# Optimization experiments

Hardware: AMD Instinct MI355X
Metric: run time of the kernel (lower is better)

## Reference

```python
import jax, jax.numpy as jnp
import numpy as np

B, S, D, W, P = 32, 512, 768, 256, 1024


def setup_inputs() -> dict:
    key = jax.random.key(0)
    k_h, k_len, k_pair, k_w1, k_w2 = jax.random.split(key, 5)
    h = jax.random.normal(k_h, (B, S, D), dtype=jnp.float32)
    # ragged word spans: each word covers 1 or 2 contiguous subwords; total <= S
    word_len = jax.random.randint(k_len, (B, W), 1, 3, dtype=jnp.int32)  # in {1,2}
    word_start = jnp.concatenate(
        [jnp.zeros((B, 1), jnp.int32), jnp.cumsum(word_len, axis=1)[:, :-1]], axis=1
    )
    # word-index pairs per configuration; -1 means "use zero embedding"
    pair_idx = jax.random.randint(k_pair, (B, P, 2), 0, W + 1, dtype=jnp.int32) - 1
    w1 = jax.random.normal(k_w1, (2 * D, 300), dtype=jnp.float32) * 0.02
    b1 = jnp.zeros((300,), jnp.float32)
    w2 = jax.random.normal(k_w2, (300, 4), dtype=jnp.float32) * 0.02
    b2 = jnp.zeros((4,), jnp.float32)
    return {"h": h, "w1": w1, "b1": b1, "w2": w2, "b2": b2,
            "word_start": word_start, "word_len": word_len, "pair_idx": pair_idx}


def reference(h, w1, b1, w2, b2, word_start, word_len, pair_idx):
    # --- mean-pool subword embeddings per word via prefix sums (segment mean) ---
    csum = jnp.cumsum(h, axis=1)                                   # [B,S,D]
    csum = jnp.concatenate([jnp.zeros_like(csum[:, :1]), csum], 1)  # [B,S+1,D]
    end = word_start + word_len                                     # [B,W]
    seg_sum = (jnp.take_along_axis(csum, end[:, :, None], axis=1)
               - jnp.take_along_axis(csum, word_start[:, :, None], axis=1))
    word_emb = seg_sum / word_len[:, :, None].astype(h.dtype)       # [B,W,D]
    # --- per-pair gather with -1 -> zero vector ---
    valid = (pair_idx >= 0)                                         # [B,P,2]
    idx = jnp.maximum(pair_idx, 0).reshape(h.shape[0], -1)          # [B,2P]
    emb = jnp.take_along_axis(word_emb, idx[:, :, None], axis=1)    # [B,2P,D]
    emb = emb.reshape(pair_idx.shape[0], pair_idx.shape[1], 2, -1)
    emb = jnp.where(valid[..., None], emb, jnp.zeros((), h.dtype))
    mlp_input = emb.reshape(-1, 2 * h.shape[-1])                    # [B*P, 2D]
    # --- tiny MLP + softmax (dropout is identity in eval) ---
    x = jnp.tanh(mlp_input @ w1 + b1)
    return jax.nn.softmax(x @ w2 + b2, axis=-1)                     # [B*P, 4]
```

## Files before the change

kernel.cpp:

```cpp
#include <hip/hip_runtime.h>
#include <cstddef>
#include <cstdint>

#define Bb   32
#define Ss   512
#define Dd   768
#define Ww   256
#define Pp   1024
#define NH   300
#define SLOT1 320
#define NPAD 640
#define Mm   (Bb * Ww)
#define ZROW 8192
#define ZOFF (ZROW * NPAD)
#define PBUF ((Mm + 1) * NPAD)
#define KH   384
#define NST  12

typedef __attribute__((ext_vector_type(8))) short bf16x8;
typedef __attribute__((ext_vector_type(4))) float f32x4;

#define GPTR(p) ((const __attribute__((address_space(1))) void*)(p))
#define LPTR(p) ((__attribute__((address_space(3))) void*)(p))

__device__ __forceinline__ unsigned short f2bf(float x) {
    unsigned u = __builtin_bit_cast(unsigned, x);
    u += 0x7fffu + ((u >> 16) & 1u);
    return (unsigned short)(u >> 16);
}
__device__ __forceinline__ float bf2f(unsigned short u) {
    return __builtin_bit_cast(float, (unsigned)u << 16);
}
__device__ __forceinline__ float fast_tanh(float x) {
    x = fminf(fmaxf(x, -15.0f), 15.0f);
    float e = __expf(2.0f * x);
    return 1.0f - 2.0f * __builtin_amdgcn_rcpf(e + 1.0f);
}

__global__ __launch_bounds__(256) void prep_kernel(
    const float* __restrict__ h, const float* __restrict__ w1,
    const int* __restrict__ word_start, const int* __restrict__ word_len,
    unsigned short* __restrict__ emb, unsigned short* __restrict__ bmatT,
    unsigned short* __restrict__ proj)
{
    const int gid    = blockIdx.x * 256 + threadIdx.x;
    const int stride = 1024 * 256;

    for (int u = gid; u < Mm * 192; u += stride) {
        const int m = u / 192;
        const int c = u - m * 192;
        const int b   = m >> 8;
        const int s0  = word_start[m];
        const int len = word_len[m];
        const float* p = h + (size_t)b * (Ss * Dd) + (size_t)s0 * Dd + c * 4;
        float4 v = *(const float4*)p;
        if (len == 2) {
            float4 v2 = *(const float4*)(p + Dd);
            v.x = (v.x + v2.x) * 0.5f;
            v.y = (v.y + v2.y) * 0.5f;
            v.z = (v.z + v2.z) * 0.5f;
            v.w = (v.w + v2.w) * 0.5f;
        }
        ushort4 o = make_ushort4(f2bf(v.x), f2bf(v.y), f2bf(v.z), f2bf(v.w));
        *(ushort4*)(emb + (size_t)m * Dd + c * 4) = o;
    }

    for (int u = gid; u < Dd * NPAD; u += stride) {
        const int k = u / NPAD;
        const int n = u - k * NPAD;
        float v = 0.0f;
        if (n < NH)                            v = w1[(size_t)k * NH + n];
        else if (n >= SLOT1 && n < SLOT1 + NH) v = w1[(size_t)(Dd + k) * NH + (n - SLOT1)];
        bmatT[(size_t)n * Dd + k] = f2bf(v);
    }

    if (gid < NPAD / 4) {
        *(ushort4*)(proj + ZOFF + gid * 4)        = make_ushort4(0, 0, 0, 0);
        *(ushort4*)(proj + PBUF + ZOFF + gid * 4) = make_ushort4(0, 0, 0, 0);
    }
}

__global__ __launch_bounds__(256) void gemm_kernel(
    const unsigned short* __restrict__ emb, const unsigned short* __restrict__ bmatT,
    unsigned short* __restrict__ proj)
{
    __shared__ bf16x8 Al[3][4][128];
    __shared__ bf16x8 Bl[3][4][128];

    const int bid = blockIdx.x;
    const int t   = threadIdx.x;

    const int swz   = (bid & 7) * 80 + (bid >> 3);
    const int kh    = swz / 320;
    const int tIdx  = swz - kh * 320;
    const int mBase = (tIdx / 5) * 128;
    const int nBase = (tIdx % 5) * 128;
    const int kOff  = kh * KH;

    const int srow = t & 127;
    const int skb8 = (t >> 7) << 3;
    const unsigned short* srcA = emb   + (size_t)(mBase + srow) * Dd + kOff + skb8;
    const unsigned short* srcB = bmatT + (size_t)(nBase + srow) * Dd + kOff + skb8;
    char* ldsA = (char*)&Al[0][0][0] + t * 16;
    char* ldsB = (char*)&Bl[0][0][0] + t * 16;

    const int lane = t & 63;
    const int w    = t >> 6;
    const int wr   = w >> 1;
    const int wc   = w & 1;
    const int fr   = lane & 15;
    const int kb   = lane >> 4;

    f32x4 acc[4][4];
#pragma unroll
    for (int i = 0; i < 4; ++i)
#pragma unroll
        for (int j = 0; j < 4; ++j)
#pragma unroll
            for (int r = 0; r < 4; ++r) acc[i][j][r] = 0.0f;

#define STAGE(c, off)                                                                          \
    __builtin_amdgcn_global_load_lds(GPTR(srcA + (off)),      LPTR(ldsA + (c) * 8192),        16, 0, 0); \
    __builtin_amdgcn_global_load_lds(GPTR(srcA + (off) + 16), LPTR(ldsA + (c) * 8192 + 4096), 16, 0, 0); \
    __builtin_amdgcn_global_load_lds(GPTR(srcB + (off)),      LPTR(ldsB + (c) * 8192),        16, 0, 0); \
    __builtin_amdgcn_global_load_lds(GPTR(srcB + (off) + 16), LPTR(ldsB + (c) * 8192 + 4096), 16, 0, 0)

#define COMPUTE(c)                                                                             \
    {                                                                                          \
        bf16x8 a[4], b[4];                                                                     \
        _Pragma("unroll")                                                                      \
        for (int mi = 0; mi < 4; ++mi) a[mi] = Al[c][kb][wr * 64 + mi * 16 + fr];              \
        _Pragma("unroll")                                                                      \
        for (int ni = 0; ni < 4; ++ni) b[ni] = Bl[c][kb][wc * 64 + ni * 16 + fr];              \
        _Pragma("unroll")                                                                      \
        for (int mi = 0; mi < 4; ++mi)                                                         \
            _Pragma("unroll")                                                                  \
            for (int ni = 0; ni < 4; ++ni)                                                     \
                acc[mi][ni] = __builtin_amdgcn_mfma_f32_16x16x32_bf16(a[mi], b[ni], acc[mi][ni], 0, 0, 0); \
    }

#define KSTEP(k, cnt)                                                     \
    asm volatile("s_waitcnt vmcnt(" #cnt ")" ::: "memory");               \
    __builtin_amdgcn_sched_barrier(0);                                    \
    __builtin_amdgcn_s_barrier();                                         \
    asm volatile("" ::: "memory");                                        \
    __builtin_amdgcn_sched_barrier(0);                                    \
    COMPUTE((k) % 3);                                                     \
    if ((k) < NST - 2) { STAGE((k + 2) % 3, (k + 2) * 32); }

    STAGE(0, 0);
    STAGE(1, 32);

    KSTEP(0, 4)  KSTEP(1, 4)  KSTEP(2, 4)  KSTEP(3, 4)
    KSTEP(4, 4)  KSTEP(5, 4)  KSTEP(6, 4)  KSTEP(7, 4)
    KSTEP(8, 4)  KSTEP(9, 4)  KSTEP(10, 4) KSTEP(11, 0)

#undef KSTEP
#undef STAGE
#undef COMPUTE

    unsigned short* projh = proj + (size_t)kh * PBUF;
    const int r0 = mBase + wr * 64 + kb * 4;
    const int c0 = nBase + wc * 64 + fr;
#pragma unroll
    for (int mi = 0; mi < 4; ++mi)
#pragma unroll
        for (int ni = 0; ni < 4; ++ni)
#pragma unroll
            for (int r = 0; r < 4; ++r)
                projh[(size_t)(r0 + mi * 16 + r) * NPAD + c0 + ni * 16] = f2bf(acc[mi][ni][r]);
}

__global__ __launch_bounds__(256) void mlp_kernel(
    const unsigned short* __restrict__ proj,
    const float* __restrict__ b1, const float* __restrict__ w2,
    const float* __restrict__ b2, const int* __restrict__ pair_idx,
    float* __restrict__ out)
{
    __shared__ float red[4][64][17];

    const int wv   = threadIdx.x >> 6;
    const int wave = blockIdx.x * 4 + wv;
    const int lane = threadIdx.x & 63;
    const int wid0 = wave * 4;
    const int b    = wid0 >> 10;
    const int rbase = b * Ww * NPAD;
    const unsigned short* proj1 = proj + PBUF;

    const int4 piA = *(const int4*)(pair_idx + wid0 * 2);
    const int4 piB = *(const int4*)(pair_idx + wid0 * 2 + 4);
    const int idx[8] = {piA.x, piA.y, piA.z, piA.w, piB.x, piB.y, piB.z, piB.w};

    int off0[4], off1[4];
#pragma unroll
    for (int p = 0; p < 4; ++p) {
        const int i0 = idx[p * 2], i1 = idx[p * 2 + 1];
        off0[p] = (i0 >= 0) ? rbase + i0 * NPAD : ZOFF;
        off1[p] = ((i1 >= 0) ? rbase + i1 * NPAD : ZOFF) + SLOT1;
    }

    unsigned short g0a[4][5], g0b[4][5], g1a[4][5], g1b[4][5];
#pragma unroll
    for (int p = 0; p < 4; ++p)
#pragma unroll
        for (int it = 0; it < 5; ++it) {
            const int j = lane + it * 64;
            g0a[p][it] = proj [(size_t)off0[p] + j];
            g0b[p][it] = proj1[(size_t)off0[p] + j];
            g1a[p][it] = proj [(size_t)off1[p] + j];
            g1b[p][it] = proj1[(size_t)off1[p] + j];
        }

    float acc[4][4];
#pragma unroll
    for (int p = 0; p < 4; ++p)
#pragma unroll
        for (int c = 0; c < 4; ++c) acc[p][c] = 0.0f;

#pragma unroll
    for (int it = 0; it < 5; ++it) {
        const int j  = lane + it * 64;
        const bool ok = (j < NH);
        const float bj = ok ? b1[j] : 0.0f;
        float4 wv4 = make_float4(0.f, 0.f, 0.f, 0.f);
        if (ok) wv4 = *(const float4*)(w2 + (size_t)j * 4);
#pragma unroll
        for (int p = 0; p < 4; ++p) {
            const float v = bj + (bf2f(g0a[p][it]) + bf2f(g0b[p][it]))
                               + (bf2f(g1a[p][it]) + bf2f(g1b[p][it]));
            const float x = ok ? fast_tanh(v) : 0.0f;
            acc[p][0] = fmaf(x, wv4.x, acc[p][0]);
            acc[p][1] = fmaf(x, wv4.y, acc[p][1]);
            acc[p][2] = fmaf(x, wv4.z, acc[p][2]);
            acc[p][3] = fmaf(x, wv4.w, acc[p][3]);
        }
    }

#pragma unroll
    for (int p = 0; p < 4; ++p)
#pragma unroll
        for (int c = 0; c < 4; ++c)
            red[wv][lane][p * 4 + c] = acc[p][c];
    __syncthreads();

    const int o = lane >> 2;
    const int g = lane & 3;
    float v = 0.0f;
#pragma unroll
    for (int i = 0; i < 16; ++i)
        v += red[wv][g * 16 + i][o];
    v += __shfl_xor(v, 1, 64);
    v += __shfl_xor(v, 2, 64);

    const int c = o & 3;
    const float l = v + b2[c];
    float mx = fmaxf(l, __shfl_xor(l, 4, 64));
    mx = fmaxf(mx, __shfl_xor(mx, 8, 64));
    const float e = __expf(l - mx);
    float s = e + __shfl_xor(e, 4, 64);
    s += __shfl_xor(s, 8, 64);
    const float r = e * __builtin_amdgcn_rcpf(s);
    if (g == 0)
        out[(size_t)(wid0 + (o >> 2)) * 4 + c] = r;
}

extern "C" void kernel_launch(void* const* d_in, const int* in_sizes, int n_in,
                              void* d_out, int out_size, void* d_ws, size_t ws_size,
                              hipStream_t stream)
{
    const float* h          = (const float*)d_in[0];
    const float* w1         = (const float*)d_in[1];
    const float* b1         = (const float*)d_in[2];
    const float* w2         = (const float*)d_in[3];
    const float* b2         = (const float*)d_in[4];
    const int*   word_start = (const int*)d_in[5];
    const int*   word_len   = (const int*)d_in[6];
    const int*   pair_idx   = (const int*)d_in[7];
    float*       out        = (float*)d_out;

    unsigned short* proj  = (unsigned short*)d_ws;
    unsigned short* emb   = (unsigned short*)((char*)d_ws + 20975616);
    unsigned short* bmatT = (unsigned short*)((char*)d_ws + 33558528);

    prep_kernel<<<dim3(1024), dim3(256), 0, stream>>>(
        h, w1, word_start, word_len, emb, bmatT, proj);
    gemm_kernel<<<dim3(640),  dim3(256), 0, stream>>>(emb, bmatT, proj);
    mlp_kernel <<<dim3(2048), dim3(256), 0, stream>>>(proj, b1, w2, b2, pair_idx, out);
}
```

Before: 55.63 us.

## Shrink GEMM to single-wave 64x64 tiles with double buffering, no barriers

Restructures the bf16 MFMA GEMM so each block is one wavefront computing a 64x64 output tile, replacing 256-thread blocks on 128x128 tiles. The LDS pipeline goes from three stages with workgroup barriers to two stages synchronised only by vmcnt waits, and the grid grows to 2560 blocks. The aim is to remove barrier overhead and raise occupancy and scheduling flexibility. In exchange, operand reuse per tile is halved, which increases global and L2 traffic.

```diff
diff --git a/kernel.cpp b/kernel.cpp
--- a/kernel.cpp
+++ b/kernel.cpp
@@ -80,36 +80,30 @@
     }
 }
 
-__global__ __launch_bounds__(256) void gemm_kernel(
+__global__ __launch_bounds__(64) void gemm_kernel(
     const unsigned short* __restrict__ emb, const unsigned short* __restrict__ bmatT,
     unsigned short* __restrict__ proj)
 {
-    __shared__ bf16x8 Al[3][4][128];
-    __shared__ bf16x8 Bl[3][4][128];
-
-    const int bid = blockIdx.x;
-    const int t   = threadIdx.x;
-
-    const int swz   = (bid & 7) * 80 + (bid >> 3);
-    const int kh    = swz / 320;
-    const int tIdx  = swz - kh * 320;
-    const int mBase = (tIdx / 5) * 128;
-    const int nBase = (tIdx % 5) * 128;
+    __shared__ bf16x8 Al[2][4][64];
+    __shared__ bf16x8 Bl[2][4][64];
+
+    const int bid  = blockIdx.x;
+    const int lane = threadIdx.x;
+
+    const int swz   = (bid & 7) * 320 + (bid >> 3);
+    const int kh    = swz / 1280;
+    const int tIdx  = swz - kh * 1280;
+    const int mBase = (tIdx / 10) * 64;
+    const int nBase = (tIdx % 10) * 64;
     const int kOff  = kh * KH;
 
-    const int srow = t & 127;
-    const int skb8 = (t >> 7) << 3;
-    const unsigned short* srcA = emb   + (size_t)(mBase + srow) * Dd + kOff + skb8;
-    const unsigned short* srcB = bmatT + (size_t)(nBase + srow) * Dd + kOff + skb8;
-    char* ldsA = (char*)&Al[0][0][0] + t * 16;
-    char* ldsB = (char*)&Bl[0][0][0] + t * 16;
-
-    const int lane = t & 63;
-    const int w    = t >> 6;
-    const int wr   = w >> 1;
-    const int wc   = w & 1;
-    const int fr   = lane & 15;
-    const int kb   = lane >> 4;
+    const unsigned short* srcA = emb   + (size_t)(mBase + lane) * Dd + kOff;
+    const unsigned short* srcB = bmatT + (size_t)(nBase + lane) * Dd + kOff;
+    char* ldsA = (char*)&Al[0][0][0] + lane * 16;
+    char* ldsB = (char*)&Bl[0][0][0] + lane * 16;
+
+    const int fr = lane & 15;
+    const int kb = lane >> 4;
 
     f32x4 acc[4][4];
 #pragma unroll
@@ -120,48 +114,48 @@
             for (int r = 0; r < 4; ++r) acc[i][j][r] = 0.0f;
 
 #define STAGE(c, off)                                                                          \
-    __builtin_amdgcn_global_load_lds(GPTR(srcA + (off)),      LPTR(ldsA + (c) * 8192),        16, 0, 0); \
-    __builtin_amdgcn_global_load_lds(GPTR(srcA + (off) + 16), LPTR(ldsA + (c) * 8192 + 4096), 16, 0, 0); \
-    __builtin_amdgcn_global_load_lds(GPTR(srcB + (off)),      LPTR(ldsB + (c) * 8192),        16, 0, 0); \
-    __builtin_amdgcn_global_load_lds(GPTR(srcB + (off) + 16), LPTR(ldsB + (c) * 8192 + 4096), 16, 0, 0)
+    _Pragma("unroll")                                                                          \
+    for (int j = 0; j < 4; ++j) {                                                              \
+        __builtin_amdgcn_global_load_lds(GPTR(srcA + (off) + j * 8),                           \
+                                         LPTR(ldsA + (c) * 4096 + j * 1024), 16, 0, 0);        \
+        __builtin_amdgcn_global_load_lds(GPTR(srcB + (off) + j * 8),                           \
+                                         LPTR(ldsB + (c) * 4096 + j * 1024), 16, 0, 0);        \
+    }
 
 #define COMPUTE(c)                                                                             \
     {                                                                                          \
         bf16x8 a[4], b[4];                                                                     \
         _Pragma("unroll")                                                                      \
-        for (int mi = 0; mi < 4; ++mi) a[mi] = Al[c][kb][wr * 64 + mi * 16 + fr];              \
+        for (int mi = 0; mi < 4; ++mi) a[mi] = Al[c][kb][mi * 16 + fr];                        \
         _Pragma("unroll")                                                                      \
-        for (int ni = 0; ni < 4; ++ni) b[ni] = Bl[c][kb][wc * 64 + ni * 16 + fr];              \
+        for (int ni = 0; ni < 4; ++ni) b[ni] = Bl[c][kb][ni * 16 + fr];                        \
         _Pragma("unroll")                                                                      \
         for (int mi = 0; mi < 4; ++mi)                                                         \
             _Pragma("unroll")                                                                  \
             for (int ni = 0; ni < 4; ++ni)                                                     \
-                acc[mi][ni] = __builtin_amdgcn_mfma_f32_16x16x32_bf16(a[mi], b[ni], acc[mi][ni], 0, 0, 0); \
+                acc[mi][ni] = __builtin_amdgcn_mfma_f32_16x16x32_bf16(a[mi], b[ni],            \
+                                                                      acc[mi][ni], 0, 0, 0);   \
     }
 
 #define KSTEP(k, cnt)                                                     \
+    if ((k) < NST - 1) { STAGE(((k) + 1) & 1, ((k) + 1) * 32); }          \
     asm volatile("s_waitcnt vmcnt(" #cnt ")" ::: "memory");               \
     __builtin_amdgcn_sched_barrier(0);                                    \
-    __builtin_amdgcn_s_barrier();                                         \
-    asm volatile("" ::: "memory");                                        \
-    __builtin_amdgcn_sched_barrier(0);                                    \
-    COMPUTE((k) % 3);                                                     \
-    if ((k) < NST - 2) { STAGE((k + 2) % 3, (k + 2) * 32); }
+    COMPUTE((k) & 1);
 
     STAGE(0, 0);
-    STAGE(1, 32);
-
-    KSTEP(0, 4)  KSTEP(1, 4)  KSTEP(2, 4)  KSTEP(3, 4)
-    KSTEP(4, 4)  KSTEP(5, 4)  KSTEP(6, 4)  KSTEP(7, 4)
-    KSTEP(8, 4)  KSTEP(9, 4)  KSTEP(10, 4) KSTEP(11, 0)
+
+    KSTEP(0, 8)  KSTEP(1, 8)  KSTEP(2, 8)  KSTEP(3, 8)
+    KSTEP(4, 8)  KSTEP(5, 8)  KSTEP(6, 8)  KSTEP(7, 8)
+    KSTEP(8, 8)  KSTEP(9, 8)  KSTEP(10, 8) KSTEP(11, 0)
 
 #undef KSTEP
 #undef STAGE
 #undef COMPUTE
 
     unsigned short* projh = proj + (size_t)kh * PBUF;
-    const int r0 = mBase + wr * 64 + kb * 4;
-    const int c0 = nBase + wc * 64 + fr;
+    const int r0 = mBase + kb * 4;
+    const int c0 = nBase + fr;
 #pragma unroll
     for (int mi = 0; mi < 4; ++mi)
 #pragma unroll
@@ -284,6 +278,6 @@
 
     prep_kernel<<<dim3(1024), dim3(256), 0, stream>>>(
         h, w1, word_start, word_len, emb, bmatT, proj);
-    gemm_kernel<<<dim3(640),  dim3(256), 0, stream>>>(emb, bmatT, proj);
+    gemm_kernel<<<dim3(2560), dim3(64),  0, stream>>>(emb, bmatT, proj);
     mlp_kernel <<<dim3(2048), dim3(256), 0, stream>>>(proj, b1, w2, b2, pair_idx, out);
 }
```

New measurement: 99.50 us. 1.79x slower.
